# Kernel tuning notes

Hardware: AMD Instinct MI355X
Metric: run time of the kernel (lower is better)

Reference implementation:

```python
import jax, jax.numpy as jnp
import numpy as np

PAD_VAL = -999
N_TYPES = 8
D_IN, D_FF, D_FFC = 512, 1024, 512
B, S = 64, 512


def setup_inputs() -> dict:
    key = jax.random.key(0)
    ks = jax.random.split(key, 6)
    sc = 0.02
    return {
        "x": jax.random.normal(ks[0], (B, S, D_IN), dtype=jnp.float32),
        "sc_types": jax.random.randint(ks[1], (B, S), 0, N_TYPES, dtype=jnp.int64),
        "W_pre": jax.random.normal(ks[2], (D_IN, D_FF), dtype=jnp.float32) * sc,
        "W_types": jax.random.normal(ks[3], (N_TYPES, D_FF, D_IN), dtype=jnp.float32) * sc,
        "W_c1": jax.random.normal(ks[4], (D_IN, D_FFC), dtype=jnp.float32) * sc,
        "W_c2": jax.random.normal(ks[5], (D_FFC, 1), dtype=jnp.float32) * sc,
    }


def reference(x, sc_types, W_pre, W_types, W_c1, W_c2):
    # flatten tokens: [B*S, d_in], [B*S]
    x = x.reshape(-1, x.shape[-1])
    t = sc_types.reshape(-1)
    # (inputs contain no PAD_VAL tokens, so the pad mask is all-True and the
    # gather x[mask] is the identity; shapes stay static)
    x_ = jax.nn.relu(x @ W_pre)                       # [N, d_ff]
    # hard type routing: select per-type MLP output for each token
    x_types = jnp.zeros_like(x)
    for i in range(N_TYPES):
        yi = jax.nn.relu(x_ @ W_types[i])             # [N, d_in]
        x_types = jnp.where((t == i)[:, None], yi, x_types)
    x = x + x_types                                    # residual combine
    h = jax.nn.relu(x @ W_c1)                          # [N, d_ffc]
    return h @ W_c2                                    # [N, 1]
```

## Files before the change

kernel.cpp:

```cpp
#include <hip/hip_runtime.h>
#include <stdint.h>

#define N_TOK 32768
#define DIN   512
#define DFF   1024
#define MPAD  33792

__device__ __forceinline__ int rotk(int k, int row) {
    return (k & ~127) + (((k & 127) + ((row & 15) << 3)) & 127);
}

typedef __attribute__((ext_vector_type(8))) short bf16x8;
typedef __attribute__((ext_vector_type(4))) float f32x4;

__device__ __forceinline__ unsigned short f2bf(float f) {
    union { float f; unsigned int u; } v; v.f = f;
    unsigned int u = v.u;
    return (unsigned short)((u + 0x7FFFu + ((u >> 16) & 1u)) >> 16);
}
__device__ __forceinline__ float bf2f(unsigned int bits) {
    union { unsigned int u; float f; } v; v.u = bits << 16; return v.f;
}
__device__ __forceinline__ unsigned int pk4_fp8(float a, float b, float c, float d) {
    int v = __builtin_amdgcn_cvt_pk_fp8_f32(a, b, 0, false);
    v = __builtin_amdgcn_cvt_pk_fp8_f32(c, d, v, true);
    return (unsigned int)v;
}
__device__ __forceinline__ unsigned char f2fp8(float a) {
    return (unsigned char)(__builtin_amdgcn_cvt_pk_fp8_f32(a, a, 0, false) & 0xFF);
}

__device__ __forceinline__ void async16(const void* g, void* l) {
    __builtin_amdgcn_global_load_lds(
        (const __attribute__((address_space(1))) void*)g,
        (__attribute__((address_space(3))) void*)l, 16, 0, 0);
}

__global__ void prep_weights_kernel(const float* __restrict__ Wp,
                                    const float* __restrict__ Wt,
                                    const float* __restrict__ Wc,
                                    unsigned char* __restrict__ Wp8,
                                    unsigned char* __restrict__ Wt8,
                                    unsigned short* __restrict__ WcT,
                                    int* __restrict__ cnt) {
    __shared__ float tile[32][33];
    const int z = blockIdx.z;
    if (z == 0 && blockIdx.x == 0 && blockIdx.y == 0 &&
        threadIdx.y == 0 && threadIdx.x < 8)
        cnt[threadIdx.x] = 0;
    const float* s; int K, N;
    if (z == 0)      { s = Wp;                          K = 512;  N = 1024; }
    else if (z <= 8) { s = Wt + (size_t)(z-1)*DIN*DFF;  K = 1024; N = 512; }
    else             { s = Wc;                          K = 512;  N = 512; }
    const int n0 = blockIdx.x * 32, k0 = blockIdx.y * 32;
    if (n0 >= N || k0 >= K) return;
    for (int i = threadIdx.y; i < 32; i += 8)
        tile[i][threadIdx.x] = s[(size_t)(k0 + i) * N + n0 + threadIdx.x];
    __syncthreads();
    if (z == 0) {
        for (int i = threadIdx.y; i < 32; i += 8) {
            int n = n0 + i;
            Wp8[(size_t)n * K + rotk(k0 + threadIdx.x, n)] = f2fp8(tile[threadIdx.x][i] * 64.f);
        }
    } else if (z <= 8) {
        unsigned char* d = Wt8 + (size_t)(z-1)*DIN*DFF;
        for (int i = threadIdx.y; i < 32; i += 8) {
            int n = n0 + i;
            d[(size_t)n * K + rotk(k0 + threadIdx.x, n)] = f2fp8(tile[threadIdx.x][i] * 64.f);
        }
    } else {
        for (int i = threadIdx.y; i < 32; i += 8)
            WcT[(size_t)(n0 + i) * K + k0 + threadIdx.x] = f2bf(tile[threadIdx.x][i]);
    }
}

__global__ void prep_tokens_kernel(const float* __restrict__ x,
                                   unsigned short* __restrict__ Xb,
                                   unsigned char* __restrict__ Xb8,
                                   const int* __restrict__ types,
                                   int* __restrict__ cnt,
                                   int* __restrict__ blockhist) {
    __shared__ int lc[8];
    const int blk = blockIdx.x, tid = threadIdx.x;
    const int i = blk * 1024 + tid * 4;
    float4 v = *(const float4*)(x + i);
    ushort4 o;
    o.x = f2bf(v.x); o.y = f2bf(v.y); o.z = f2bf(v.z); o.w = f2bf(v.w);
    *(ushort4*)(Xb + i) = o;
    const int row = i >> 9;
    const int k   = i & 511;
    *(unsigned int*)(Xb8 + (size_t)row * DIN + rotk(k, row)) = pk4_fp8(v.x, v.y, v.z, v.w);
    if (blk < 64) {
        if (tid < 8) lc[tid] = 0;
        __syncthreads();
        atomicAdd(&lc[types[blk * 512 + tid]], 1);
        atomicAdd(&lc[types[blk * 512 + 256 + tid]], 1);
        __syncthreads();
        if (tid < 8) {
            atomicAdd(&cnt[tid], lc[tid]);
            blockhist[blk * 8 + tid] = lc[tid];
        }
    }
}

__global__ void scatter_kernel(const int* __restrict__ types,
                               const int* __restrict__ cnt,
                               const int* __restrict__ blockhist,
                               int* __restrict__ perm,
                               int* __restrict__ invperm,
                               float* __restrict__ outz) {
    __shared__ int base[8];
    __shared__ int fill[8];
    const int blk = blockIdx.x;
    const int tid = threadIdx.x;
    const int i = blk * 512 + tid;
    outz[i] = 0.f;
    if (tid < 8) {
        int off = 0, pob = 0;
        #pragma unroll
        for (int b = 0; b < 8; b++) {
            if (b == tid) pob = off;
            off += ((cnt[b] + 127) >> 7) << 7;
        }
        int pre = 0;
        for (int j = 0; j < blk; j++) pre += blockhist[j * 8 + tid];
        base[tid] = pob + pre;
        fill[tid] = 0;
    }
    __syncthreads();
    const int t = types[i];
    const int r = atomicAdd(&fill[t], 1);
    const int p = base[t] + r;
    perm[p] = i;
    invperm[i] = p;
}

__global__ void perm_pad_kernel(int* __restrict__ perm) {
    perm[blockIdx.x * 256 + threadIdx.x] = -1;
}

template <int MODE>
__global__ __launch_bounds__(256, 4)
void gemm_fp8_kernel(const unsigned char* __restrict__ A,
                     const unsigned char* __restrict__ B,
                     void* __restrict__ Cout,
                     const unsigned short* __restrict__ xres,
                     const int* __restrict__ perm,
                     const int* __restrict__ invperm,
                     const int* __restrict__ cnt,
                     int K, int ldA) {
    __shared__ unsigned char As[128 * 128];
    __shared__ unsigned char Bs[128 * 128];
    __shared__ int ptile[128];

    const int tid  = threadIdx.x;
    const int wave = tid >> 6;
    const int lane = tid & 63;
    const int quad = lane >> 4;
    const int tl   = lane & 15;
    const int m0 = blockIdx.y * 128;
    const int n0 = blockIdx.x * 128;
    const int wm = (wave & 1) * 64;
    const int wn = (wave >> 1) * 64;

    const unsigned char* Bp = B;
    if constexpr (MODE == 1) {
        int bsel = 0, total = 0;
        #pragma unroll
        for (int i = 0; i < 8; i++) {
            if (i > 0 && m0 >= total) bsel = i;
            total += ((cnt[i] + 127) >> 7) << 7;
        }
        if (m0 >= total) return;
        Bp = B + (size_t)bsel * (DIN * DFF);
        if (tid < 128) ptile[tid] = perm[m0 + tid];
    } else {
        if (tid < 128) ptile[tid] = invperm[m0 + tid];
    }

    f32x4 acc[4][4];
    #pragma unroll
    for (int i = 0; i < 4; i++)
        #pragma unroll
        for (int j = 0; j < 4; j++)
            acc[i][j] = (f32x4){0.f, 0.f, 0.f, 0.f};

    for (int k0 = 0; k0 < K; k0 += 128) {
        __syncthreads();
        #pragma unroll
        for (int i = 0; i < 4; i++) {
            const int c   = (i * 4 + wave) * 64 + lane;
            const int row = c >> 3;
            const int j   = c & 7;
            async16(A + (size_t)(m0 + row) * ldA + k0 + j * 16, (char*)As + (size_t)c * 16);
        }
        #pragma unroll
        for (int i = 0; i < 4; i++) {
            const int c   = (i * 4 + wave) * 64 + lane;
            const int row = c >> 3;
            const int j   = c & 7;
            async16(Bp + (size_t)(n0 + row) * K + k0 + j * 16, (char*)Bs + (size_t)c * 16);
        }
        __syncthreads();

        #pragma unroll
        for (int ks = 0; ks < 4; ks++) {
            long af[4], bfr[4];
            const int o = (ks * 32 + quad * 8 + tl * 8) & 127;
            #pragma unroll
            for (int t = 0; t < 4; t++)
                af[t] = *(const long*)(As + (wm + t * 16 + tl) * 128 + o);
            #pragma unroll
            for (int t = 0; t < 4; t++)
                bfr[t] = *(const long*)(Bs + (wn + t * 16 + tl) * 128 + o);
            #pragma unroll
            for (int mt = 0; mt < 4; mt++)
                #pragma unroll
                for (int nt = 0; nt < 4; nt++)
                    acc[mt][nt] = __builtin_amdgcn_mfma_f32_16x16x32_fp8_fp8(
                        bfr[nt], af[mt], acc[mt][nt], 0, 0, 0);
        }
    }

    if constexpr (MODE == 0) {
        unsigned char* C8 = (unsigned char*)Cout;
        #pragma unroll
        for (int mt = 0; mt < 4; mt++) {
            const int p = ptile[wm + mt * 16 + tl];
            const size_t rowbase = (size_t)p * DFF;
            #pragma unroll
            for (int nt = 0; nt < 4; nt++) {
                const int off = wn + nt * 16 + quad * 4;
                unsigned int pk = pk4_fp8(fmaxf(acc[mt][nt][0], 0.f) * 0.125f,
                                          fmaxf(acc[mt][nt][1], 0.f) * 0.125f,
                                          fmaxf(acc[mt][nt][2], 0.f) * 0.125f,
                                          fmaxf(acc[mt][nt][3], 0.f) * 0.125f);
                const int phys = (off & ~127) + (((off & 127) + ((p & 15) << 3)) & 127);
                *(unsigned int*)(C8 + rowbase + n0 + phys) = pk;
            }
        }
    } else {
        unsigned short* Cb = (unsigned short*)Cout;
        #pragma unroll
        for (int mt = 0; mt < 4; mt++) {
            int tok = ptile[wm + mt * 16 + tl];
            if (tok < 0) continue;
            const size_t rowbase = (size_t)tok * DIN;
            #pragma unroll
            for (int nt = 0; nt < 4; nt++) {
                const int ncol = n0 + wn + nt * 16 + quad * 4;
                ushort4 rv = *(const ushort4*)(xres + rowbase + ncol);
                ushort4 o;
                o.x = f2bf(bf2f(rv.x) + fmaxf(acc[mt][nt][0], 0.f) * 0.001953125f);
                o.y = f2bf(bf2f(rv.y) + fmaxf(acc[mt][nt][1], 0.f) * 0.001953125f);
                o.z = f2bf(bf2f(rv.z) + fmaxf(acc[mt][nt][2], 0.f) * 0.001953125f);
                o.w = f2bf(bf2f(rv.w) + fmaxf(acc[mt][nt][3], 0.f) * 0.001953125f);
                *(ushort4*)(Cb + rowbase + ncol) = o;
            }
        }
    }
}

__global__ __launch_bounds__(512, 4)
void gemm3_kernel(const unsigned short* __restrict__ A,
                  const unsigned short* __restrict__ B,
                  const float* __restrict__ w2,
                  float* __restrict__ outp,
                  int K, int ldA) {
    __shared__ unsigned short As[128 * 64];
    __shared__ unsigned short Bs[256 * 64];

    const int tid  = threadIdx.x;
    const int wave = tid >> 6;
    const int lane = tid & 63;
    const int quad = lane >> 4;
    const int tl   = lane & 15;
    const int m0 = blockIdx.y * 128;
    const int n0 = blockIdx.x * 256;
    const int wm = (wave & 1) * 64;
    const int wn = (wave >> 1) * 64;

    f32x4 acc[4][4];
    #pragma unroll
    for (int i = 0; i < 4; i++)
        #pragma unroll
        for (int j = 0; j < 4; j++)
            acc[i][j] = (f32x4){0.f, 0.f, 0.f, 0.f};

    for (int k0 = 0; k0 < K; k0 += 64) {
        __syncthreads();
        #pragma unroll
        for (int i = 0; i < 2; i++) {
            const int c   = (i * 8 + wave) * 64 + lane;
            const int row = c >> 3;
            const int gj  = (c & 7) ^ (row & 7);
            async16(A + (size_t)(m0 + row) * ldA + k0 + gj * 8, (char*)As + (size_t)c * 16);
        }
        #pragma unroll
        for (int i = 0; i < 4; i++) {
            const int c   = (i * 8 + wave) * 64 + lane;
            const int row = c >> 3;
            const int gj  = (c & 7) ^ (row & 7);
            async16(B + (size_t)(n0 + row) * K + k0 + gj * 8, (char*)Bs + (size_t)c * 16);
        }
        __syncthreads();

        #pragma unroll
        for (int ks = 0; ks < 2; ks++) {
            bf16x8 af[4], bfr[4];
            const int jc = ks * 4 + quad;
            #pragma unroll
            for (int t = 0; t < 4; t++) {
                const int r = wm + t * 16 + tl;
                af[t] = *(const bf16x8*)(As + (r * 8 + (jc ^ (r & 7))) * 8);
            }
            #pragma unroll
            for (int t = 0; t < 4; t++) {
                const int r = wn + t * 16 + tl;
                bfr[t] = *(const bf16x8*)(Bs + (r * 8 + (jc ^ (r & 7))) * 8);
            }
            #pragma unroll
            for (int mt = 0; mt < 4; mt++)
                #pragma unroll
                for (int nt = 0; nt < 4; nt++)
                    acc[mt][nt] = __builtin_amdgcn_mfma_f32_16x16x32_bf16(
                        bfr[nt], af[mt], acc[mt][nt], 0, 0, 0);
        }
    }

    float4 w2v[4];
    #pragma unroll
    for (int nt = 0; nt < 4; nt++)
        w2v[nt] = *(const float4*)(w2 + n0 + wn + nt * 16 + quad * 4);
    #pragma unroll
    for (int mt = 0; mt < 4; mt++) {
        float s = 0.f;
        #pragma unroll
        for (int nt = 0; nt < 4; nt++) {
            s += fmaxf(acc[mt][nt][0], 0.f) * w2v[nt].x;
            s += fmaxf(acc[mt][nt][1], 0.f) * w2v[nt].y;
            s += fmaxf(acc[mt][nt][2], 0.f) * w2v[nt].z;
            s += fmaxf(acc[mt][nt][3], 0.f) * w2v[nt].w;
        }
        s += __shfl_down(s, 32);
        s += __shfl_down(s, 16);
        if (lane < 16) atomicAdd(&outp[m0 + wm + mt * 16 + lane], s);
    }
}

extern "C" void kernel_launch(void* const* d_in, const int* in_sizes, int n_in,
                              void* d_out, int out_size, void* d_ws, size_t ws_size,
                              hipStream_t stream) {
    const float* x      = (const float*)d_in[0];
    const int*   types  = (const int*)d_in[1];
    const float* W_pre  = (const float*)d_in[2];
    const float* W_types= (const float*)d_in[3];
    const float* W_c1   = (const float*)d_in[4];
    const float* W_c2   = (const float*)d_in[5];
    float* out = (float*)d_out;

    char* ws = (char*)d_ws;
    unsigned short* Xb  = (unsigned short*)(ws);
    unsigned char*  Xff8= (unsigned char*)(ws + 33554432ull);
    unsigned char*  Xb8 = (unsigned char*)(ws + 68157440ull);
    unsigned char*  Wp8 = (unsigned char*)(ws + 84934656ull);
    unsigned char*  Wt8 = (unsigned char*)(ws + 85458944ull);
    unsigned short* WcT = (unsigned short*)(ws + 89653248ull);
    int* perm           = (int*)(ws + 90177536ull);
    int* invperm        = (int*)(ws + 90312704ull);
    int* cnt            = (int*)(ws + 90443776ull);
    int* blockhist      = cnt + 16;

    prep_weights_kernel<<<dim3(32, 32, 10), dim3(32, 8), 0, stream>>>(
        W_pre, W_types, W_c1, Wp8, Wt8, WcT, cnt);
    perm_pad_kernel<<<MPAD / 256, 256, 0, stream>>>(perm);
    prep_tokens_kernel<<<N_TOK * DIN / 1024, 256, 0, stream>>>(x, Xb, Xb8, types, cnt, blockhist);
    scatter_kernel<<<64, 512, 0, stream>>>(types, cnt, blockhist, perm, invperm, out);

    gemm_fp8_kernel<0><<<dim3(DFF / 128, N_TOK / 128), 256, 0, stream>>>(
        Xb8, Wp8, Xff8, nullptr, nullptr, invperm, cnt, 512, 512);
    gemm_fp8_kernel<1><<<dim3(DIN / 128, MPAD / 128), 256, 0, stream>>>(
        Xff8, Wt8, Xb, Xb, perm, nullptr, cnt, 1024, 1024);
    gemm3_kernel<<<dim3(DIN / 256, N_TOK / 128), 512, 0, stream>>>(
        Xb, WcT, W_c2, out, 512, 512);
}
```

Measured before the change: 235.4 us.

## Use 32x32x64 scaled FP8 MFMA and fuse prep kernels into one launch

The two FP8 GEMMs move from 16x16x32 fp8 MFMA to the gfx950 mfma_scale 32x32x64 f8f6f4 instruction, which does more work per instruction and uses fewer LDS fragment loads per FLOP, with new fragment and epilogue index mapping. The weight-prep, token-prep and perm-pad kernels are merged into one launch to cut launch overhead. The global count atomics are dropped: the scatter kernel now computes type totals and segment offsets from the block histogram and publishes them for the routing GEMM. The new lane mapping and swizzle handling must match the MFMA layout exactly or results will be wrong.

New measurement: 292.2 us. 1.24x slower.

```diff
diff --git a/kernel.cpp b/kernel.cpp
--- a/kernel.cpp
+++ b/kernel.cpp
@@ -12,6 +12,8 @@
 
 typedef __attribute__((ext_vector_type(8))) short bf16x8;
 typedef __attribute__((ext_vector_type(4))) float f32x4;
+typedef __attribute__((ext_vector_type(8))) int i32x8;
+typedef __attribute__((ext_vector_type(16))) float f32x16;
 
 __device__ __forceinline__ unsigned short f2bf(float f) {
     union { float f; unsigned int u; } v; v.f = f;
@@ -36,96 +38,107 @@
         (__attribute__((address_space(3))) void*)l, 16, 0, 0);
 }
 
-__global__ void prep_weights_kernel(const float* __restrict__ Wp,
-                                    const float* __restrict__ Wt,
-                                    const float* __restrict__ Wc,
-                                    unsigned char* __restrict__ Wp8,
-                                    unsigned char* __restrict__ Wt8,
-                                    unsigned short* __restrict__ WcT,
-                                    int* __restrict__ cnt) {
+__global__ void prep_kernel(const float* __restrict__ x,
+                            unsigned short* __restrict__ Xb,
+                            unsigned char* __restrict__ Xb8,
+                            const int* __restrict__ types,
+                            int* __restrict__ blockhist,
+                            const float* __restrict__ Wp,
+                            const float* __restrict__ Wt,
+                            const float* __restrict__ Wc,
+                            unsigned char* __restrict__ Wp8,
+                            unsigned char* __restrict__ Wt8,
+                            unsigned short* __restrict__ WcT,
+                            int* __restrict__ perm) {
     __shared__ float tile[32][33];
-    const int z = blockIdx.z;
-    if (z == 0 && blockIdx.x == 0 && blockIdx.y == 0 &&
-        threadIdx.y == 0 && threadIdx.x < 8)
-        cnt[threadIdx.x] = 0;
-    const float* s; int K, N;
-    if (z == 0)      { s = Wp;                          K = 512;  N = 1024; }
-    else if (z <= 8) { s = Wt + (size_t)(z-1)*DIN*DFF;  K = 1024; N = 512; }
-    else             { s = Wc;                          K = 512;  N = 512; }
-    const int n0 = blockIdx.x * 32, k0 = blockIdx.y * 32;
-    if (n0 >= N || k0 >= K) return;
-    for (int i = threadIdx.y; i < 32; i += 8)
-        tile[i][threadIdx.x] = s[(size_t)(k0 + i) * N + n0 + threadIdx.x];
-    __syncthreads();
-    if (z == 0) {
-        for (int i = threadIdx.y; i < 32; i += 8) {
-            int n = n0 + i;
-            Wp8[(size_t)n * K + rotk(k0 + threadIdx.x, n)] = f2fp8(tile[threadIdx.x][i] * 64.f);
-        }
-    } else if (z <= 8) {
-        unsigned char* d = Wt8 + (size_t)(z-1)*DIN*DFF;
-        for (int i = threadIdx.y; i < 32; i += 8) {
-            int n = n0 + i;
-            d[(size_t)n * K + rotk(k0 + threadIdx.x, n)] = f2fp8(tile[threadIdx.x][i] * 64.f);
+    __shared__ int lc[8];
+    const int b = blockIdx.x, tid = threadIdx.x;
+    if (b < 16384) {
+        const int i = b * 1024 + tid * 4;
+        float4 v = *(const float4*)(x + i);
+        ushort4 o;
+        o.x = f2bf(v.x); o.y = f2bf(v.y); o.z = f2bf(v.z); o.w = f2bf(v.w);
+        *(ushort4*)(Xb + i) = o;
+        const int row = i >> 9;
+        const int k   = i & 511;
+        *(unsigned int*)(Xb8 + (size_t)row * DIN + rotk(k, row)) = pk4_fp8(v.x, v.y, v.z, v.w);
+        if (b < 64) {
+            if (tid < 8) lc[tid] = 0;
+            __syncthreads();
+            atomicAdd(&lc[types[b * 512 + tid]], 1);
+            atomicAdd(&lc[types[b * 512 + 256 + tid]], 1);
+            __syncthreads();
+            if (tid < 8) blockhist[b * 8 + tid] = lc[tid];
+        }
+    } else if (b < 26624) {
+        const int r = b - 16384;
+        const int z = r >> 10;
+        const int bx = r & 31, by = (r >> 5) & 31;
+        const int tx = tid & 31, ty = tid >> 5;
+        const float* s; int K, N;
+        if (z == 0)      { s = Wp;                          K = 512;  N = 1024; }
+        else if (z <= 8) { s = Wt + (size_t)(z-1)*DIN*DFF;  K = 1024; N = 512; }
+        else             { s = Wc;                          K = 512;  N = 512; }
+        const int n0 = bx * 32, k0 = by * 32;
+        if (n0 >= N || k0 >= K) return;
+        for (int i = ty; i < 32; i += 8)
+            tile[i][tx] = s[(size_t)(k0 + i) * N + n0 + tx];
+        __syncthreads();
+        if (z == 0) {
+            for (int i = ty; i < 32; i += 8) {
+                int n = n0 + i;
+                Wp8[(size_t)n * K + rotk(k0 + tx, n)] = f2fp8(tile[tx][i] * 64.f);
+            }
+        } else if (z <= 8) {
+            unsigned char* d = Wt8 + (size_t)(z-1)*DIN*DFF;
+            for (int i = ty; i < 32; i += 8) {
+                int n = n0 + i;
+                d[(size_t)n * K + rotk(k0 + tx, n)] = f2fp8(tile[tx][i] * 64.f);
+            }
+        } else {
+            for (int i = ty; i < 32; i += 8)
+                WcT[(size_t)(n0 + i) * K + k0 + tx] = f2bf(tile[tx][i]);
         }
     } else {
-        for (int i = threadIdx.y; i < 32; i += 8)
-            WcT[(size_t)(n0 + i) * K + k0 + threadIdx.x] = f2bf(tile[threadIdx.x][i]);
-    }
-}
-
-__global__ void prep_tokens_kernel(const float* __restrict__ x,
-                                   unsigned short* __restrict__ Xb,
-                                   unsigned char* __restrict__ Xb8,
-                                   const int* __restrict__ types,
-                                   int* __restrict__ cnt,
-                                   int* __restrict__ blockhist) {
-    __shared__ int lc[8];
-    const int blk = blockIdx.x, tid = threadIdx.x;
-    const int i = blk * 1024 + tid * 4;
-    float4 v = *(const float4*)(x + i);
-    ushort4 o;
-    o.x = f2bf(v.x); o.y = f2bf(v.y); o.z = f2bf(v.z); o.w = f2bf(v.w);
-    *(ushort4*)(Xb + i) = o;
-    const int row = i >> 9;
-    const int k   = i & 511;
-    *(unsigned int*)(Xb8 + (size_t)row * DIN + rotk(k, row)) = pk4_fp8(v.x, v.y, v.z, v.w);
-    if (blk < 64) {
-        if (tid < 8) lc[tid] = 0;
-        __syncthreads();
-        atomicAdd(&lc[types[blk * 512 + tid]], 1);
-        atomicAdd(&lc[types[blk * 512 + 256 + tid]], 1);
-        __syncthreads();
-        if (tid < 8) {
-            atomicAdd(&cnt[tid], lc[tid]);
-            blockhist[blk * 8 + tid] = lc[tid];
-        }
+        perm[(b - 26624) * 256 + tid] = -1;
     }
 }
 
 __global__ void scatter_kernel(const int* __restrict__ types,
-                               const int* __restrict__ cnt,
                                const int* __restrict__ blockhist,
                                int* __restrict__ perm,
                                int* __restrict__ invperm,
-                               float* __restrict__ outz) {
-    __shared__ int base[8];
-    __shared__ int fill[8];
+                               float* __restrict__ outz,
+                               int* __restrict__ po_out) {
+    __shared__ int tots[8], base[8], fill[8];
     const int blk = blockIdx.x;
     const int tid = threadIdx.x;
     const int i = blk * 512 + tid;
     outz[i] = 0.f;
+    int pre = 0;
+    if (tid < 8) {
+        int total = 0;
+        for (int j = 0; j < 64; j++) {
+            int v = blockhist[j * 8 + tid];
+            if (j < blk) pre += v;
+            total += v;
+        }
+        tots[tid] = total;
+    }
+    __syncthreads();
     if (tid < 8) {
         int off = 0, pob = 0;
         #pragma unroll
-        for (int b = 0; b < 8; b++) {
-            if (b == tid) pob = off;
-            off += ((cnt[b] + 127) >> 7) << 7;
-        }
-        int pre = 0;
-        for (int j = 0; j < blk; j++) pre += blockhist[j * 8 + tid];
+        for (int t2 = 0; t2 < 8; t2++) {
+            if (t2 == tid) pob = off;
+            off += ((tots[t2] + 127) >> 7) << 7;
+        }
         base[tid] = pob + pre;
         fill[tid] = 0;
+        if (blk == 0) {
+            po_out[tid] = pob;
+            if (tid == 0) po_out[8] = off;
+        }
     }
     __syncthreads();
     const int t = types[i];
@@ -135,19 +148,14 @@
     invperm[i] = p;
 }
 
-__global__ void perm_pad_kernel(int* __restrict__ perm) {
-    perm[blockIdx.x * 256 + threadIdx.x] = -1;
-}
-
 template <int MODE>
 __global__ __launch_bounds__(256, 4)
 void gemm_fp8_kernel(const unsigned char* __restrict__ A,
                      const unsigned char* __restrict__ B,
                      void* __restrict__ Cout,
                      const unsigned short* __restrict__ xres,
-                     const int* __restrict__ perm,
-                     const int* __restrict__ invperm,
-                     const int* __restrict__ cnt,
+                     const int* __restrict__ pmap,
+                     const int* __restrict__ po,
                      int K, int ldA) {
     __shared__ unsigned char As[128 * 128];
     __shared__ unsigned char Bs[128 * 128];
@@ -156,8 +164,8 @@
     const int tid  = threadIdx.x;
     const int wave = tid >> 6;
     const int lane = tid & 63;
-    const int quad = lane >> 4;
-    const int tl   = lane & 15;
+    const int m32  = lane & 31;
+    const int kh   = lane >> 5;
     const int m0 = blockIdx.y * 128;
     const int n0 = blockIdx.x * 128;
     const int wm = (wave & 1) * 64;
@@ -165,25 +173,22 @@
 
     const unsigned char* Bp = B;
     if constexpr (MODE == 1) {
-        int bsel = 0, total = 0;
-        #pragma unroll
-        for (int i = 0; i < 8; i++) {
-            if (i > 0 && m0 >= total) bsel = i;
-            total += ((cnt[i] + 127) >> 7) << 7;
-        }
-        if (m0 >= total) return;
+        if (m0 >= po[8]) return;
+        int bsel = 0;
+        #pragma unroll
+        for (int i = 1; i < 8; i++) bsel += (m0 >= po[i]) ? 1 : 0;
         Bp = B + (size_t)bsel * (DIN * DFF);
-        if (tid < 128) ptile[tid] = perm[m0 + tid];
-    } else {
-        if (tid < 128) ptile[tid] = invperm[m0 + tid];
-    }
-
-    f32x4 acc[4][4];
+    }
+    if (tid < 128) ptile[tid] = pmap[m0 + tid];
+
+    f32x16 acc[2][2];
     #pragma unroll
-    for (int i = 0; i < 4; i++)
-        #pragma unroll
-        for (int j = 0; j < 4; j++)
-            acc[i][j] = (f32x4){0.f, 0.f, 0.f, 0.f};
+    for (int i = 0; i < 2; i++)
+        #pragma unroll
+        for (int j = 0; j < 2; j++)
+            #pragma unroll
+            for (int c = 0; c < 16; c++)
+                acc[i][j][c] = 0.f;
 
     for (int k0 = 0; k0 < K; k0 += 128) {
         __syncthreads();
@@ -204,58 +209,81 @@
         __syncthreads();
 
         #pragma unroll
-        for (int ks = 0; ks < 4; ks++) {
-            long af[4], bfr[4];
-            const int o = (ks * 32 + quad * 8 + tl * 8) & 127;
-            #pragma unroll
-            for (int t = 0; t < 4; t++)
-                af[t] = *(const long*)(As + (wm + t * 16 + tl) * 128 + o);
-            #pragma unroll
-            for (int t = 0; t < 4; t++)
-                bfr[t] = *(const long*)(Bs + (wn + t * 16 + tl) * 128 + o);
-            #pragma unroll
-            for (int mt = 0; mt < 4; mt++)
-                #pragma unroll
-                for (int nt = 0; nt < 4; nt++)
-                    acc[mt][nt] = __builtin_amdgcn_mfma_f32_16x16x32_fp8_fp8(
-                        bfr[nt], af[mt], acc[mt][nt], 0, 0, 0);
+        for (int ks = 0; ks < 2; ks++) {
+            const int j0 = ks * 64 + kh * 32;
+            i32x8 af[2], bfr[2];
+            #pragma unroll
+            for (int mt = 0; mt < 2; mt++) {
+                const int r = wm + mt * 32 + m32;
+                const int rot = (r & 15) << 3;
+                long* pa = (long*)&af[mt];
+                #pragma unroll
+                for (int u = 0; u < 4; u++)
+                    pa[u] = *(const long*)(As + r * 128 + ((j0 + u * 8 + rot) & 127));
+            }
+            #pragma unroll
+            for (int nt = 0; nt < 2; nt++) {
+                const int r = wn + nt * 32 + m32;
+                const int rot = (r & 15) << 3;
+                long* pb = (long*)&bfr[nt];
+                #pragma unroll
+                for (int u = 0; u < 4; u++)
+                    pb[u] = *(const long*)(Bs + r * 128 + ((j0 + u * 8 + rot) & 127));
+            }
+            #pragma unroll
+            for (int mt = 0; mt < 2; mt++)
+                #pragma unroll
+                for (int nt = 0; nt < 2; nt++)
+                    acc[mt][nt] = __builtin_amdgcn_mfma_scale_f32_32x32x64_f8f6f4(
+                        bfr[nt], af[mt], acc[mt][nt],
+                        0, 0,
+                        0, 0x7F,
+                        0, 0x7F);
         }
     }
 
     if constexpr (MODE == 0) {
         unsigned char* C8 = (unsigned char*)Cout;
         #pragma unroll
-        for (int mt = 0; mt < 4; mt++) {
-            const int p = ptile[wm + mt * 16 + tl];
+        for (int mt = 0; mt < 2; mt++) {
+            const int p = ptile[wm + mt * 32 + m32];
             const size_t rowbase = (size_t)p * DFF;
-            #pragma unroll
-            for (int nt = 0; nt < 4; nt++) {
-                const int off = wn + nt * 16 + quad * 4;
-                unsigned int pk = pk4_fp8(fmaxf(acc[mt][nt][0], 0.f) * 0.125f,
-                                          fmaxf(acc[mt][nt][1], 0.f) * 0.125f,
-                                          fmaxf(acc[mt][nt][2], 0.f) * 0.125f,
-                                          fmaxf(acc[mt][nt][3], 0.f) * 0.125f);
-                const int phys = (off & ~127) + (((off & 127) + ((p & 15) << 3)) & 127);
-                *(unsigned int*)(C8 + rowbase + n0 + phys) = pk;
+            const int prot = (p & 15) << 3;
+            #pragma unroll
+            for (int nt = 0; nt < 2; nt++) {
+                #pragma unroll
+                for (int r2 = 0; r2 < 4; r2++) {
+                    const int off = n0 + wn + nt * 32 + r2 * 8 + kh * 4;
+                    unsigned int pk = pk4_fp8(
+                        fmaxf(acc[mt][nt][r2 * 4 + 0], 0.f) * 0.125f,
+                        fmaxf(acc[mt][nt][r2 * 4 + 1], 0.f) * 0.125f,
+                        fmaxf(acc[mt][nt][r2 * 4 + 2], 0.f) * 0.125f,
+                        fmaxf(acc[mt][nt][r2 * 4 + 3], 0.f) * 0.125f);
+                    const int phys = (off & ~127) + (((off & 127) + prot) & 127);
+                    *(unsigned int*)(C8 + rowbase + phys) = pk;
+                }
             }
         }
     } else {
         unsigned short* Cb = (unsigned short*)Cout;
         #pragma unroll
-        for (int mt = 0; mt < 4; mt++) {
-            int tok = ptile[wm + mt * 16 + tl];
+        for (int mt = 0; mt < 2; mt++) {
+            int tok = ptile[wm + mt * 32 + m32];
             if (tok < 0) continue;
             const size_t rowbase = (size_t)tok * DIN;
             #pragma unroll
-            for (int nt = 0; nt < 4; nt++) {
-                const int ncol = n0 + wn + nt * 16 + quad * 4;
-                ushort4 rv = *(const ushort4*)(xres + rowbase + ncol);
-                ushort4 o;
-                o.x = f2bf(bf2f(rv.x) + fmaxf(acc[mt][nt][0], 0.f) * 0.001953125f);
-                o.y = f2bf(bf2f(rv.y) + fmaxf(acc[mt][nt][1], 0.f) * 0.001953125f);
-                o.z = f2bf(bf2f(rv.z) + fmaxf(acc[mt][nt][2], 0.f) * 0.001953125f);
-                o.w = f2bf(bf2f(rv.w) + fmaxf(acc[mt][nt][3], 0.f) * 0.001953125f);
-                *(ushort4*)(Cb + rowbase + ncol) = o;
+            for (int nt = 0; nt < 2; nt++) {
+                #pragma unroll
+                for (int r2 = 0; r2 < 4; r2++) {
+                    const int ncol = n0 + wn + nt * 32 + r2 * 8 + kh * 4;
+                    ushort4 rv = *(const ushort4*)(xres + rowbase + ncol);
+                    ushort4 o;
+                    o.x = f2bf(bf2f(rv.x) + fmaxf(acc[mt][nt][r2*4+0], 0.f) * 0.001953125f);
+                    o.y = f2bf(bf2f(rv.y) + fmaxf(acc[mt][nt][r2*4+1], 0.f) * 0.001953125f);
+                    o.z = f2bf(bf2f(rv.z) + fmaxf(acc[mt][nt][r2*4+2], 0.f) * 0.001953125f);
+                    o.w = f2bf(bf2f(rv.w) + fmaxf(acc[mt][nt][r2*4+3], 0.f) * 0.001953125f);
+                    *(ushort4*)(Cb + rowbase + ncol) = o;
+                }
             }
         }
     }
@@ -368,19 +396,16 @@
     unsigned short* WcT = (unsigned short*)(ws + 89653248ull);
     int* perm           = (int*)(ws + 90177536ull);
     int* invperm        = (int*)(ws + 90312704ull);
-    int* cnt            = (int*)(ws + 90443776ull);
-    int* blockhist      = cnt + 16;
-
-    prep_weights_kernel<<<dim3(32, 32, 10), dim3(32, 8), 0, stream>>>(
-        W_pre, W_types, W_c1, Wp8, Wt8, WcT, cnt);
-    perm_pad_kernel<<<MPAD / 256, 256, 0, stream>>>(perm);
-    prep_tokens_kernel<<<N_TOK * DIN / 1024, 256, 0, stream>>>(x, Xb, Xb8, types, cnt, blockhist);
-    scatter_kernel<<<64, 512, 0, stream>>>(types, cnt, blockhist, perm, invperm, out);
-
+    int* po             = (int*)(ws + 90443776ull);
+    int* blockhist      = po + 16;
+
+    prep_kernel<<<26756, 256, 0, stream>>>(x, Xb, Xb8, types, blockhist,
+                                           W_pre, W_types, W_c1, Wp8, Wt8, WcT, perm);
+    scatter_kernel<<<64, 512, 0, stream>>>(types, blockhist, perm, invperm, out, po);
     gemm_fp8_kernel<0><<<dim3(DFF / 128, N_TOK / 128), 256, 0, stream>>>(
-        Xb8, Wp8, Xff8, nullptr, nullptr, invperm, cnt, 512, 512);
+        Xb8, Wp8, Xff8, nullptr, invperm, nullptr, 512, 512);
     gemm_fp8_kernel<1><<<dim3(DIN / 128, MPAD / 128), 256, 0, stream>>>(
-        Xff8, Wt8, Xb, Xb, perm, nullptr, cnt, 1024, 1024);
+        Xff8, Wt8, Xb, Xb, perm, po, 1024, 1024);
     gemm3_kernel<<<dim3(DIN / 256, N_TOK / 128), 512, 0, stream>>>(
         Xb, WcT, W_c2, out, 512, 512);
 }
```
